# Kernel tuning notes

Hardware: AMD Instinct MI355X
Metric: run time of the kernel (lower is better)

The kernel has to match this reference:

```python
import jax, jax.numpy as jnp
import numpy as np

N_SRC = 100_000
N_NODES = 1_000_000
N_NEIGH = 20
RAW_DIM = 256
NEIGH_DIM = 128
MSG_DIM = 128


def setup_inputs() -> dict:
    key = jax.random.key(0)
    ks = jax.random.split(key, 8)
    s = 0.05
    return {
        "raw_messages": jax.random.normal(ks[0], (N_SRC, RAW_DIM), dtype=jnp.float32),
        "neighbors": jax.random.randint(ks[1], (N_SRC, N_NEIGH), 0, N_NODES, dtype=jnp.int64),
        "memory": jax.random.normal(ks[2], (N_NODES, NEIGH_DIM), dtype=jnp.float32),
        "W1": jax.random.normal(ks[3], (RAW_DIM, RAW_DIM // 2), dtype=jnp.float32) * s,
        "b1": jnp.zeros((RAW_DIM // 2,), dtype=jnp.float32),
        "W2": jax.random.normal(ks[4], (RAW_DIM // 2, MSG_DIM), dtype=jnp.float32) * s,
        "b2": jnp.zeros((MSG_DIM,), dtype=jnp.float32),
        "Wn": jax.random.normal(ks[5], (NEIGH_DIM, MSG_DIM), dtype=jnp.float32) * s,
        "bn": jnp.zeros((MSG_DIM,), dtype=jnp.float32),
    }


def reference(raw_messages, neighbors, memory, W1, b1, W2, b2, Wn, bn):
    # Gather neighbor memories: [N, K, D_neigh]
    neighbor_memories = memory[neighbors]
    # Mean-pool over the K sampled neighbors: [N, D_neigh]
    neighbor_agg = neighbor_memories.mean(axis=1)
    # message_sum MLP: Linear -> ReLU -> Linear -> ReLU
    h = jax.nn.relu(raw_messages @ W1 + b1)
    a = jax.nn.relu(h @ W2 + b2)
    # neighbor_sum MLP: Linear -> ReLU
    b = jax.nn.relu(neighbor_agg @ Wn + bn)
    return a + b
```

## Files before the change

kernel.cpp:

```cpp
#include <hip/hip_runtime.h>

#define N_SRC   100000
#define N_NEIGH 20
#define DRAW    256
#define DH      128
#define DMSG    128
#define DNEI    128
#define LDS_PAD 8

typedef __bf16 bf16x8 __attribute__((ext_vector_type(8)));
typedef float  floatx4 __attribute__((ext_vector_type(4)));

__global__ void convert_weights(const float* __restrict__ W1,
                                const float* __restrict__ W2,
                                const float* __restrict__ Wn,
                                __bf16* __restrict__ W1t,
                                __bf16* __restrict__ W2t,
                                __bf16* __restrict__ Wnt) {
    int i = blockIdx.x * 256 + threadIdx.x;
    if (i < 32768) {
        int n = i >> 8, k = i & 255;
        W1t[i] = (__bf16)W1[k * 128 + n];
    } else if (i < 49152) {
        int j = i - 32768;
        int n = j >> 7, k = j & 127;
        W2t[j] = (__bf16)W2[k * 128 + n];
    } else {
        int j = i - 49152;
        int n = j >> 7, k = j & 127;
        Wnt[j] = (__bf16)Wn[k * 128 + n];
    }
}

__global__ __launch_bounds__(256)
void fused_kernel(const float* __restrict__ raw,
                  const int*   __restrict__ neigh,
                  const float* __restrict__ memv,
                  const float* __restrict__ b1,
                  const float* __restrict__ b2,
                  const float* __restrict__ bn,
                  const __bf16* __restrict__ W1t,
                  const __bf16* __restrict__ W2t,
                  const __bf16* __restrict__ Wnt,
                  float* __restrict__ out) {
    __shared__ __bf16 agg [64][DNEI + LDS_PAD];
    __shared__ __bf16 hbuf[64][DH   + LDS_PAD];

    const int tid = threadIdx.x;
    const int s0  = blockIdx.x * 64;

    {
        const int grp = tid >> 5;
        const int l32 = tid & 31;
        for (int sl = grp; sl < 64; sl += 8) {
            const int s = s0 + sl;
            float4 acc = make_float4(0.f, 0.f, 0.f, 0.f);
            if (s < N_SRC) {
                int myidx = 0;
                if (l32 < N_NEIGH) myidx = neigh[s * N_NEIGH + l32];
                #pragma unroll
                for (int n = 0; n < N_NEIGH; ++n) {
                    int idx = __shfl(myidx, n, 32);
                    const float4* row =
                        reinterpret_cast<const float4*>(memv + (size_t)idx * DNEI);
                    float4 v = row[l32];
                    acc.x += v.x; acc.y += v.y; acc.z += v.z; acc.w += v.w;
                }
                const float inv = 1.0f / N_NEIGH;
                acc.x *= inv; acc.y *= inv; acc.z *= inv; acc.w *= inv;
            }
            __bf16* dst = &agg[sl][l32 * 4];
            dst[0] = (__bf16)acc.x; dst[1] = (__bf16)acc.y;
            dst[2] = (__bf16)acc.z; dst[3] = (__bf16)acc.w;
        }
    }

    const int lane = tid & 63;
    const int wave = tid >> 6;
    const int mr   = lane & 15;
    const int quad = lane >> 4;

    {
        int rowg = s0 + wave * 16 + mr;
        int rowc = rowg < N_SRC ? rowg : N_SRC - 1;
        const float* ar = raw + (size_t)rowc * DRAW;

        floatx4 acc[8];
        #pragma unroll
        for (int nt = 0; nt < 8; ++nt) { floatx4 z = {0.f,0.f,0.f,0.f}; acc[nt] = z; }

        #pragma unroll
        for (int kk = 0; kk < DRAW; kk += 32) {
            const int kb = kk + quad * 8;
            float4 a0 = *reinterpret_cast<const float4*>(ar + kb);
            float4 a1 = *reinterpret_cast<const float4*>(ar + kb + 4);
            bf16x8 af;
            af[0]=(__bf16)a0.x; af[1]=(__bf16)a0.y; af[2]=(__bf16)a0.z; af[3]=(__bf16)a0.w;
            af[4]=(__bf16)a1.x; af[5]=(__bf16)a1.y; af[6]=(__bf16)a1.z; af[7]=(__bf16)a1.w;
            #pragma unroll
            for (int nt = 0; nt < 8; ++nt) {
                bf16x8 bf = *reinterpret_cast<const bf16x8*>(
                    W1t + (nt * 16 + mr) * DRAW + kb);
                acc[nt] = __builtin_amdgcn_mfma_f32_16x16x32_bf16(af, bf, acc[nt], 0, 0, 0);
            }
        }
        #pragma unroll
        for (int nt = 0; nt < 8; ++nt) {
            const int col  = nt * 16 + mr;
            const float bias = b1[col];
            #pragma unroll
            for (int r = 0; r < 4; ++r) {
                int mrow = wave * 16 + quad * 4 + r;
                float v = acc[nt][r] + bias;
                hbuf[mrow][col] = (__bf16)(v > 0.f ? v : 0.f);
            }
        }
    }

    __syncthreads();

    {
        floatx4 acc2[8], acc3[8];
        #pragma unroll
        for (int nt = 0; nt < 8; ++nt) {
            floatx4 z = {0.f,0.f,0.f,0.f}; acc2[nt] = z; acc3[nt] = z;
        }

        #pragma unroll
        for (int kk = 0; kk < DH; kk += 32) {
            const int kb = kk + quad * 8;
            bf16x8 af2 = *reinterpret_cast<const bf16x8*>(&hbuf[wave * 16 + mr][kb]);
            bf16x8 af3 = *reinterpret_cast<const bf16x8*>(&agg [wave * 16 + mr][kb]);
            #pragma unroll
            for (int nt = 0; nt < 8; ++nt) {
                bf16x8 bw2 = *reinterpret_cast<const bf16x8*>(
                    W2t + (nt * 16 + mr) * DH + kb);
                acc2[nt] = __builtin_amdgcn_mfma_f32_16x16x32_bf16(af2, bw2, acc2[nt], 0, 0, 0);
                bf16x8 bw3 = *reinterpret_cast<const bf16x8*>(
                    Wnt + (nt * 16 + mr) * DNEI + kb);
                acc3[nt] = __builtin_amdgcn_mfma_f32_16x16x32_bf16(af3, bw3, acc3[nt], 0, 0, 0);
            }
        }

        #pragma unroll
        for (int nt = 0; nt < 8; ++nt) {
            const int col = nt * 16 + mr;
            const float bb2 = b2[col];
            const float bbn = bn[col];
            #pragma unroll
            for (int r = 0; r < 4; ++r) {
                int rowl = wave * 16 + quad * 4 + r;
                int rowg = s0 + rowl;
                if (rowg < N_SRC) {
                    float va = acc2[nt][r] + bb2; va = va > 0.f ? va : 0.f;
                    float vb = acc3[nt][r] + bbn; vb = vb > 0.f ? vb : 0.f;
                    out[(size_t)rowg * DMSG + col] = va + vb;
                }
            }
        }
    }
}

extern "C" void kernel_launch(void* const* d_in, const int* in_sizes, int n_in,
                              void* d_out, int out_size, void* d_ws, size_t ws_size,
                              hipStream_t stream) {
    const float* raw   = (const float*)d_in[0];
    const int*   neigh = (const int*)  d_in[1];
    const float* memv  = (const float*)d_in[2];
    const float* W1    = (const float*)d_in[3];
    const float* b1    = (const float*)d_in[4];
    const float* W2    = (const float*)d_in[5];
    const float* b2    = (const float*)d_in[6];
    const float* Wn    = (const float*)d_in[7];
    const float* bn    = (const float*)d_in[8];
    float* out = (float*)d_out;

    __bf16* W1t = (__bf16*)d_ws;
    __bf16* W2t = W1t + 32768;
    __bf16* Wnt = W2t + 16384;

    convert_weights<<<dim3(256), dim3(256), 0, stream>>>(W1, W2, Wn, W1t, W2t, Wnt);

    const int nblocks = (N_SRC + 63) / 64;
    fused_kernel<<<dim3(nblocks), dim3(256), 0, stream>>>(
        raw, neigh, memv, b1, b2, bn, W1t, W2t, Wnt, out);
}
```

Measured before the change: 888.2 us.

## Split neighbor gather-mean into its own wave-per-row kernel before MLP

Measured after the change: 900.6 us. About the same (+1.4%).

```diff
diff --git a/kernel.cpp b/kernel.cpp
--- a/kernel.cpp
+++ b/kernel.cpp
@@ -33,56 +33,63 @@
 }
 
 __global__ __launch_bounds__(256)
-void fused_kernel(const float* __restrict__ raw,
-                  const int*   __restrict__ neigh,
-                  const float* __restrict__ memv,
-                  const float* __restrict__ b1,
-                  const float* __restrict__ b2,
-                  const float* __restrict__ bn,
-                  const __bf16* __restrict__ W1t,
-                  const __bf16* __restrict__ W2t,
-                  const __bf16* __restrict__ Wnt,
-                  float* __restrict__ out) {
-    __shared__ __bf16 agg [64][DNEI + LDS_PAD];
-    __shared__ __bf16 hbuf[64][DH   + LDS_PAD];
-
-    const int tid = threadIdx.x;
-    const int s0  = blockIdx.x * 64;
-
-    {
-        const int grp = tid >> 5;
-        const int l32 = tid & 31;
-        for (int sl = grp; sl < 64; sl += 8) {
-            const int s = s0 + sl;
-            float4 acc = make_float4(0.f, 0.f, 0.f, 0.f);
-            if (s < N_SRC) {
-                int myidx = 0;
-                if (l32 < N_NEIGH) myidx = neigh[s * N_NEIGH + l32];
-                #pragma unroll
-                for (int n = 0; n < N_NEIGH; ++n) {
-                    int idx = __shfl(myidx, n, 32);
-                    const float4* row =
-                        reinterpret_cast<const float4*>(memv + (size_t)idx * DNEI);
-                    float4 v = row[l32];
-                    acc.x += v.x; acc.y += v.y; acc.z += v.z; acc.w += v.w;
-                }
-                const float inv = 1.0f / N_NEIGH;
-                acc.x *= inv; acc.y *= inv; acc.z *= inv; acc.w *= inv;
-            }
-            __bf16* dst = &agg[sl][l32 * 4];
-            dst[0] = (__bf16)acc.x; dst[1] = (__bf16)acc.y;
-            dst[2] = (__bf16)acc.z; dst[3] = (__bf16)acc.w;
-        }
-    }
-
+void gather_mean(const int*   __restrict__ neigh,
+                 const float* __restrict__ memv,
+                 float*       __restrict__ agg) {
+    const int wid  = blockIdx.x * 4 + (threadIdx.x >> 6);
+    const int lane = threadIdx.x & 63;
+    if (wid >= N_SRC) return;
+
+    int myidx = 0;
+    if (lane < N_NEIGH) myidx = neigh[wid * N_NEIGH + lane];
+
+    float2 v[N_NEIGH];
+    #pragma unroll
+    for (int n = 0; n < N_NEIGH; ++n) {
+        int idx = __shfl(myidx, n, 64);
+        v[n] = reinterpret_cast<const float2*>(memv + (size_t)idx * DNEI)[lane];
+    }
+    float sx = 0.f, sy = 0.f;
+    #pragma unroll
+    for (int n = 0; n < N_NEIGH; ++n) { sx += v[n].x; sy += v[n].y; }
+    const float inv = 1.0f / N_NEIGH;
+    float2 r; r.x = sx * inv; r.y = sy * inv;
+    reinterpret_cast<float2*>(agg + (size_t)wid * DNEI)[lane] = r;
+}
+
+__global__ __launch_bounds__(256)
+void mlp_kernel(const float* __restrict__ raw,
+                const float* __restrict__ agg,
+                const float* __restrict__ b1,
+                const float* __restrict__ b2,
+                const float* __restrict__ bn,
+                const __bf16* __restrict__ W1t,
+                const __bf16* __restrict__ W2t,
+                const __bf16* __restrict__ Wnt,
+                float* __restrict__ out) {
+    __shared__ __bf16 hbuf[64][DH + LDS_PAD];
+
+    const int tid  = threadIdx.x;
+    const int s0   = blockIdx.x * 64;
     const int lane = tid & 63;
     const int wave = tid >> 6;
     const int mr   = lane & 15;
     const int quad = lane >> 4;
 
+    const int rowg = s0 + wave * 16 + mr;
+    const int rowc = rowg < N_SRC ? rowg : N_SRC - 1;
+
+    float4 ag[8];
     {
-        int rowg = s0 + wave * 16 + mr;
-        int rowc = rowg < N_SRC ? rowg : N_SRC - 1;
+        const float* ar3 = agg + (size_t)rowc * DNEI;
+        #pragma unroll
+        for (int i = 0; i < 4; ++i) {
+            ag[2 * i]     = *reinterpret_cast<const float4*>(ar3 + i * 32 + quad * 8);
+            ag[2 * i + 1] = *reinterpret_cast<const float4*>(ar3 + i * 32 + quad * 8 + 4);
+        }
+    }
+
+    {
         const float* ar = raw + (size_t)rowc * DRAW;
 
         floatx4 acc[8];
@@ -129,8 +136,14 @@
         #pragma unroll
         for (int kk = 0; kk < DH; kk += 32) {
             const int kb = kk + quad * 8;
+            const int i  = kk >> 5;
             bf16x8 af2 = *reinterpret_cast<const bf16x8*>(&hbuf[wave * 16 + mr][kb]);
-            bf16x8 af3 = *reinterpret_cast<const bf16x8*>(&agg [wave * 16 + mr][kb]);
+            bf16x8 af3;
+            {
+                float4 g0 = ag[2 * i], g1 = ag[2 * i + 1];
+                af3[0]=(__bf16)g0.x; af3[1]=(__bf16)g0.y; af3[2]=(__bf16)g0.z; af3[3]=(__bf16)g0.w;
+                af3[4]=(__bf16)g1.x; af3[5]=(__bf16)g1.y; af3[6]=(__bf16)g1.z; af3[7]=(__bf16)g1.w;
+            }
             #pragma unroll
             for (int nt = 0; nt < 8; ++nt) {
                 bf16x8 bw2 = *reinterpret_cast<const bf16x8*>(
@@ -150,11 +163,11 @@
             #pragma unroll
             for (int r = 0; r < 4; ++r) {
                 int rowl = wave * 16 + quad * 4 + r;
-                int rowg = s0 + rowl;
-                if (rowg < N_SRC) {
+                int rg   = s0 + rowl;
+                if (rg < N_SRC) {
                     float va = acc2[nt][r] + bb2; va = va > 0.f ? va : 0.f;
                     float vb = acc3[nt][r] + bbn; vb = vb > 0.f ? vb : 0.f;
-                    out[(size_t)rowg * DMSG + col] = va + vb;
+                    out[(size_t)rg * DMSG + col] = va + vb;
                 }
             }
         }
@@ -181,7 +194,10 @@
 
     convert_weights<<<dim3(256), dim3(256), 0, stream>>>(W1, W2, Wn, W1t, W2t, Wnt);
 
+    float* agg = out;
+    gather_mean<<<dim3((N_SRC + 3) / 4), dim3(256), 0, stream>>>(neigh, memv, agg);
+
     const int nblocks = (N_SRC + 63) / 64;
-    fused_kernel<<<dim3(nblocks), dim3(256), 0, stream>>>(
-        raw, neigh, memv, b1, b2, bn, W1t, W2t, Wnt, out);
-}
+    mlp_kernel<<<dim3(nblocks), dim3(256), 0, stream>>>(
+        raw, agg, b1, b2, bn, W1t, W2t, Wnt, out);
+}
```
